# Performance work log

Measured on AMD Instinct MI355X. Metric: run time of the kernel, lower is better.

Reference implementation:

```python
import jax, jax.numpy as jnp
import numpy as np

DT = 0.005
BETA = 0.9
THR = 0.5
TAU_MIN = 0.02
TAU_STEP = 0.03
TAU_R = 0.002
SLOPE = 25.0  # snntorch fast_sigmoid default surrogate slope

@jax.custom_vjp
def spike_fn(x):
    return (x > 0).astype(x.dtype)

def _spike_fwd(x):
    return spike_fn(x), x

def _spike_bwd(x, g):
    return (g / (SLOPE * jnp.abs(x) + 1.0) ** 2,)

spike_fn.defvjp(_spike_fwd, _spike_bwd)

def setup_inputs() -> dict:
    key = jax.random.key(0)
    ks = jax.random.split(key, 8)
    T, NIN, H, NOUT, P = 1000, 4, 4096, 2, 16
    inv_sqrt_h = 1.0 / np.sqrt(H).astype(np.float32)
    return {
        "x": jax.random.normal(ks[0], (T, NIN + 2, 1), jnp.float32),
        "noise": jax.random.normal(ks[1], (T, H, 1), jnp.float32),
        "Win": jax.random.normal(ks[2], (H, NIN + 2), jnp.float32),
        "Wout": jax.random.normal(ks[3], (NOUT, H), jnp.float32) * inv_sqrt_h,
        "pin": jax.random.normal(ks[4], (H, P), jnp.float32) * inv_sqrt_h,
        "pout": jax.random.normal(ks[5], (H, P), jnp.float32) * inv_sqrt_h,
        "l": jax.random.normal(ks[6], (P,), jnp.float32) * inv_sqrt_h,
        "sigmoid_tau_d": jax.random.normal(ks[7], (H, 1), jnp.float32),
    }

def reference(x, noise, Win, Wout, pin, pout, l, sigmoid_tau_d):
    H = Win.shape[0]
    tau_d = jax.nn.sigmoid(sigmoid_tau_d) * TAU_STEP + TAU_MIN   # [H,1]
    Wr = (l * pin) @ pout.T                                      # [H,H] low-rank recurrent matrix
    decay_r = jnp.exp(jnp.asarray(-DT / TAU_R, x.dtype))         # scalar
    decay_d = jnp.exp(-DT / tau_d)                               # [H,1]
    s_gain = DT / (tau_d * TAU_R)                                # [H,1]

    def step(carry, inp):
        mem, r, s = carry
        xi, ni = inp
        I = Win @ xi + Wr @ r + ni / 10.0                        # [H,1]
        # snntorch Leaky, reset_mechanism='subtract': reset from incoming mem (detached)
        reset = jax.lax.stop_gradient(spike_fn(mem - THR))
        mem = BETA * mem + I - reset * THR
        spk = spike_fn(mem - THR)
        s = s * decay_r + s_gain * spk
        r = decay_d * r + DT * s
        return (mem, r, s), r

    z = jnp.zeros((H, 1), x.dtype)
    _, R = jax.lax.scan(step, (z, z, z), (x, noise))             # R: [T,H,1]
    y = jnp.einsum('oh,thj->toj', Wout, R)                       # [T,O,1]
    return y
```

## Files before the change

kernel.cpp:

```cpp
#include <hip/hip_runtime.h>
#include <math.h>

#define KB       4
#define NTHREADS 256
#define NW       4
#define HID      4096
#define HB       (HID / KB)
#define NPT      4
#define TT       1000
#define PP       16
#define SLOTW    32

#define BETA 0.9f
#define THRV 0.5f
#define DTV  0.005f

template<int CTRL>
__device__ __forceinline__ float dppx(float v) {
    return __int_as_float(__builtin_amdgcn_update_dpp(
        0, __float_as_int(v), CTRL, 0xF, 0xF, true));
}

__device__ __forceinline__ unsigned long long AL(const unsigned long long* p) {
    return __hip_atomic_load(p, __ATOMIC_RELAXED, __HIP_MEMORY_SCOPE_AGENT);
}
__device__ __forceinline__ void AS(unsigned long long* p, unsigned long long v) {
    __hip_atomic_store(p, v, __ATOMIC_RELAXED, __HIP_MEMORY_SCOPE_AGENT);
}

__global__ __launch_bounds__(NTHREADS, 1)
void snn_kernel(const float* __restrict__ x,
                const float* __restrict__ noise,
                const float* __restrict__ Win,
                const float* __restrict__ Wout,
                const float* __restrict__ pin,
                const float* __restrict__ pout,
                const float* __restrict__ lvec,
                const float* __restrict__ stdv,
                float* __restrict__ ypart,
                unsigned long long* __restrict__ slots)
{
    const int b    = blockIdx.x;
    const int tid  = threadIdx.x;
    const int wave = tid >> 6;
    const int lane = tid & 63;
    const int h0   = b * HB + tid * NPT;

    const bool lb0 = (lane & 1) != 0;
    const bool lb1 = (lane & 2) != 0;
    const bool lb2 = (lane & 4) != 0;
    const bool lb3 = (lane & 8) != 0;

    const int rbA = (b == 0) ? 1 : 0;
    const int rbB = (b <= 1) ? 2 : 1;
    const int rbC = (b <= 2) ? 3 : 2;

    __shared__ float part[NW][20];
    __shared__ float ubuf[NW][16];

    float lv[PP];
    #pragma unroll
    for (int p = 0; p < PP; p += 4) {
        float4 t4 = *(const float4*)&lvec[p];
        lv[p] = t4.x; lv[p+1] = t4.y; lv[p+2] = t4.z; lv[p+3] = t4.w;
    }
    float pl[NPT][PP], po[NPT][PP];
    #pragma unroll
    for (int j = 0; j < NPT; ++j) {
        #pragma unroll
        for (int p = 0; p < PP; p += 4) {
            float4 a = *(const float4*)&pin[(h0+j)*PP + p];
            pl[j][p]   = a.x*lv[p];   pl[j][p+1] = a.y*lv[p+1];
            pl[j][p+2] = a.z*lv[p+2]; pl[j][p+3] = a.w*lv[p+3];
            float4 e4 = *(const float4*)&pout[(h0+j)*PP + p];
            po[j][p]   = e4.x; po[j][p+1] = e4.y;
            po[j][p+2] = e4.z; po[j][p+3] = e4.w;
        }
    }
    float win[NPT][6];
    #pragma unroll
    for (int j = 0; j < NPT; ++j) {
        const float2* wr = (const float2*)&Win[(h0+j)*6];
        float2 wA = wr[0], wB = wr[1], wC = wr[2];
        win[j][0]=wA.x; win[j][1]=wA.y; win[j][2]=wB.x;
        win[j][3]=wB.y; win[j][4]=wC.x; win[j][5]=wC.y;
    }
    float4 woa = *(const float4*)&Wout[h0];
    float4 wob = *(const float4*)&Wout[HID + h0];

    float4 sd4 = *(const float4*)&stdv[h0];
    float dd[NPT], sg[NPT];
    {
        float sdv[4] = { sd4.x, sd4.y, sd4.z, sd4.w };
        #pragma unroll
        for (int j = 0; j < NPT; ++j) {
            float sig = 1.f / (1.f + expf(-sdv[j]));
            float tau = sig * 0.03f + 0.02f;
            dd[j] = expf(-DTV / tau);
            sg[j] = DTV / (tau * 0.002f);
        }
    }
    const float DECAY_R = expf(-2.5f);
    const float DTE     = DTV * DECAY_R;

    float mem[NPT], rr[NPT], ss[NPT];
    float pre[NPT], rlin[NPT], slin[NPT];
    float palin[PP], yalin = 0.f, yblin = 0.f;
    #pragma unroll
    for (int j = 0; j < NPT; ++j) { mem[j]=0.f; rr[j]=0.f; ss[j]=0.f; }
    #pragma unroll
    for (int p = 0; p < PP; ++p) palin[p] = 0.f;

    const float2* x2 = (const float2*)x;
    float4 nz = *(const float4*)&noise[h0];
    float2 xa = x2[0], xb = x2[1], xc = x2[2];

    float uu[16];
    #pragma unroll
    for (int p = 0; p < 16; ++p) uu[p] = 0.f;

    for (int t = 0; t <= TT; ++t) {
        const int par = t & 1;

        float bs = 0.f;
        if (t > 0) {
            if (lane < 18) {
                bs = (part[0][lane] + part[1][lane])
                   + (part[2][lane] + part[3][lane]);
            }
            if (wave == 0) {
                if (lane < 16) {
                    if (t < TT) {
                        union { float f; unsigned u; } cv; cv.f = bs;
                        unsigned long long pk =
                            ((unsigned long long)(unsigned)t << 32)
                          | (unsigned long long)cv.u;
                        AS(&slots[(size_t)(par*KB + b)*SLOTW + lane], pk);
                    }
                } else if (lane < 18) {
                    ypart[(size_t)b*(2*TT) + (t-1)*2 + (lane-16)] = bs;
                }
            }
        }

        if (t < TT) {
            float nzv[4] = { nz.x, nz.y, nz.z, nz.w };
            #pragma unroll
            for (int j = 0; j < NPT; ++j) {
                float xw = win[j][0]*xa.x + win[j][1]*xa.y
                         + win[j][2]*xb.x + win[j][3]*xb.y
                         + win[j][4]*xc.x + win[j][5]*xc.y;
                float rst = (mem[j] - THRV > 0.f) ? THRV : 0.f;
                pre[j]  = BETA*mem[j] + xw + nzv[j] / 10.0f - rst;
                rlin[j] = dd[j]*rr[j] + DTE*ss[j];
                slin[j] = DECAY_R*ss[j];
            }
            #pragma unroll
            for (int p = 0; p < PP; ++p)
                palin[p] = (po[0][p]*rlin[0] + po[1][p]*rlin[1])
                         + (po[2][p]*rlin[2] + po[3][p]*rlin[3]);
            yalin = (woa.x*rlin[0]+woa.y*rlin[1]) + (woa.z*rlin[2]+woa.w*rlin[3]);
            yblin = (wob.x*rlin[0]+wob.y*rlin[1]) + (wob.z*rlin[2]+wob.w*rlin[3]);
        }

        if (t > 0 && t < TT) {
            const size_t sb = (size_t)par * KB;
            float f0 = 0.f, f1 = 0.f, f2 = 0.f;
            if (lane < 16) {
                const unsigned long long* pa_ = &slots[(sb + rbA)*SLOTW + lane];
                const unsigned long long* pb_ = &slots[(sb + rbB)*SLOTW + lane];
                const unsigned long long* pc_ = &slots[(sb + rbC)*SLOTW + lane];
                unsigned long long va, vb, vc;
                int sp = 0;
                do {
                    va = AL(pa_); vb = AL(pb_); vc = AL(pc_);
                } while ((((unsigned)(va >> 32) != (unsigned)t) |
                          ((unsigned)(vb >> 32) != (unsigned)t) |
                          ((unsigned)(vc >> 32) != (unsigned)t)) &&
                         ++sp < (1 << 20));
                union { unsigned u; float f; } c0, c1, c2;
                c0.u = (unsigned)va; c1.u = (unsigned)vb; c2.u = (unsigned)vc;
                f0 = c0.f; f1 = c1.f; f2 = c2.f;
            }
            float total = (b < 2) ? ((bs + f0) + (f1 + f2))
                                  : ((f0 + f1) + (f2 + bs));
            if (lane < 16) ubuf[wave][lane] = total;
            float4 u0 = *(const float4*)&ubuf[wave][0];
            float4 u1 = *(const float4*)&ubuf[wave][4];
            float4 u2 = *(const float4*)&ubuf[wave][8];
            float4 u3 = *(const float4*)&ubuf[wave][12];
            uu[0]=u0.x; uu[1]=u0.y; uu[2]=u0.z; uu[3]=u0.w;
            uu[4]=u1.x; uu[5]=u1.y; uu[6]=u1.z; uu[7]=u1.w;
            uu[8]=u2.x; uu[9]=u2.y; uu[10]=u2.z; uu[11]=u2.w;
            uu[12]=u3.x; uu[13]=u3.y; uu[14]=u3.z; uu[15]=u3.w;
        }

        if (t < TT) {
            if (t < TT - 1) {
                const int tn = t + 1;
                nz = *(const float4*)&noise[tn * HID + h0];
                xa = x2[tn*3]; xb = x2[tn*3+1]; xc = x2[tn*3+2];
            }

            float rs[NPT];
            #pragma unroll
            for (int j = 0; j < NPT; ++j) {
                float ra  = pl[j][0]*uu[0];
                float rb_ = pl[j][8]*uu[8];
                #pragma unroll
                for (int p = 1; p < 8; ++p) {
                    ra  += pl[j][p]*uu[p];
                    rb_ += pl[j][p+8]*uu[p+8];
                }
                mem[j] = pre[j] + (ra + rb_);
                bool spk = (mem[j] - THRV > 0.f);
                float rspk = spk ? DTV*sg[j] : 0.f;
                ss[j] = slin[j] + (spk ? sg[j] : 0.f);
                rr[j] = rlin[j] + rspk;
                rs[j] = rspk;
            }
            float pa[18];
            #pragma unroll
            for (int p = 0; p < PP; ++p)
                pa[p] = palin[p] + ((po[0][p]*rs[0] + po[1][p]*rs[1])
                                 +  (po[2][p]*rs[2] + po[3][p]*rs[3]));
            pa[16] = yalin + ((woa.x*rs[0]+woa.y*rs[1]) + (woa.z*rs[2]+woa.w*rs[3]));
            pa[17] = yblin + ((wob.x*rs[0]+wob.y*rs[1]) + (wob.z*rs[2]+wob.w*rs[3]));

            float a1[8], yv;
            #pragma unroll
            for (int k = 0; k < 8; ++k) {
                float keep = lb0 ? pa[2*k+1] : pa[2*k];
                float send = lb0 ? pa[2*k]   : pa[2*k+1];
                a1[k] = keep + dppx<0xB1>(send);
            }
            {
                float keep = lb0 ? pa[17] : pa[16];
                float send = lb0 ? pa[16] : pa[17];
                yv = keep + dppx<0xB1>(send);
            }
            float a2[4];
            #pragma unroll
            for (int k = 0; k < 4; ++k) {
                float keep = lb1 ? a1[2*k+1] : a1[2*k];
                float send = lb1 ? a1[2*k]   : a1[2*k+1];
                a2[k] = keep + dppx<0x4E>(send);
            }
            yv += dppx<0x4E>(yv);
            float a3[2];
            #pragma unroll
            for (int k = 0; k < 2; ++k) {
                float keep = lb2 ? a2[2*k+1] : a2[2*k];
                float send = lb2 ? a2[2*k]   : a2[2*k+1];
                a3[k] = keep + __shfl_xor(send, 4, 64);
            }
            yv += __shfl_xor(yv, 4, 64);
            float uv;
            {
                float keep = lb3 ? a3[1] : a3[0];
                float send = lb3 ? a3[0] : a3[1];
                uv = keep + dppx<0x128>(send);
            }
            yv += dppx<0x128>(yv);
            uv += __shfl_xor(uv, 16, 64);
            uv += __shfl_xor(uv, 32, 64);
            yv += __shfl_xor(yv, 16, 64);
            yv += __shfl_xor(yv, 32, 64);

            if (lane < 18) part[wave][lane] = (lane < 16) ? uv : yv;
            __syncthreads();
        }
    }
}

__global__ void ysum_kernel(const float* __restrict__ yp, float* __restrict__ out) {
    int i = blockIdx.x * blockDim.x + threadIdx.x;
    if (i < 2 * TT) {
        float a = yp[i];
        float b = yp[2*TT + i];
        float c = yp[2*2*TT + i];
        float d = yp[3*2*TT + i];
        out[i] = (a + b) + (c + d);
    }
}

extern "C" void kernel_launch(void* const* d_in, const int* in_sizes, int n_in,
                              void* d_out, int out_size, void* d_ws, size_t ws_size,
                              hipStream_t stream)
{
    const float* x     = (const float*)d_in[0];
    const float* noise = (const float*)d_in[1];
    const float* Win   = (const float*)d_in[2];
    const float* Wout  = (const float*)d_in[3];
    const float* pin   = (const float*)d_in[4];
    const float* pout  = (const float*)d_in[5];
    const float* l     = (const float*)d_in[6];
    const float* stdv  = (const float*)d_in[7];
    float* out = (float*)d_out;
    unsigned long long* slots = (unsigned long long*)d_ws;
    float* ypart = (float*)((char*)d_ws + 4096);

    hipLaunchKernelGGL(snn_kernel, dim3(KB), dim3(NTHREADS), 0, stream,
                       x, noise, Win, Wout, pin, pout, l, stdv,
                       ypart, slots);
    hipLaunchKernelGGL(ysum_kernel, dim3((2*TT + 255)/256), dim3(256), 0, stream,
                       ypart, out);
}
```

Measured before the change: 1.611 ms.

## Exchange cross-block partials through L2 with a fallback to device-scope atomics

Launches 32 blocks and keeps only every eighth, so the four working blocks likely land on the same XCD and share an L2. Partial sums are written to two slot arrays: a plain store for L2 and an agent-scope atomic store. Readers poll the L2 copy with a buffer_inv plus plain loads and a bounded spin, and fall back permanently to the atomic copy if that times out. The aim is lower latency per step for the inter-block synchronisation, at the cost of relying on an undocumented block-to-XCD placement and extra stores.

Measured after the change: 1.689 ms. 1.05x slower.

```diff
diff --git a/kernel.cpp b/kernel.cpp
--- a/kernel.cpp
+++ b/kernel.cpp
@@ -2,6 +2,7 @@
 #include <math.h>
 
 #define KB       4
+#define NBOOT    32
 #define NTHREADS 256
 #define NW       4
 #define HID      4096
@@ -26,6 +27,23 @@
 }
 __device__ __forceinline__ void AS(unsigned long long* p, unsigned long long v) {
     __hip_atomic_store(p, v, __ATOMIC_RELAXED, __HIP_MEMORY_SCOPE_AGENT);
+}
+__device__ __forceinline__ void st64_plain(unsigned long long* p, unsigned long long v) {
+    asm volatile("global_store_dwordx2 %0, %1, off" :: "v"(p), "v"(v) : "memory");
+}
+__device__ __forceinline__ void inv_ld3(const unsigned long long* p0,
+                                        const unsigned long long* p1,
+                                        const unsigned long long* p2,
+                                        unsigned long long& v0,
+                                        unsigned long long& v1,
+                                        unsigned long long& v2) {
+    asm volatile("buffer_inv sc0\n\t"
+                 "global_load_dwordx2 %0, %3, off\n\t"
+                 "global_load_dwordx2 %1, %4, off\n\t"
+                 "global_load_dwordx2 %2, %5, off\n\t"
+                 "s_waitcnt vmcnt(0)"
+                 : "=&v"(v0), "=&v"(v1), "=&v"(v2)
+                 : "v"(p0), "v"(p1), "v"(p2) : "memory");
 }
 
 __global__ __launch_bounds__(NTHREADS, 1)
@@ -38,9 +56,12 @@
                 const float* __restrict__ lvec,
                 const float* __restrict__ stdv,
                 float* __restrict__ ypart,
-                unsigned long long* __restrict__ slots)
+                unsigned long long* __restrict__ slotsL2,
+                unsigned long long* __restrict__ slotsAG)
 {
-    const int b    = blockIdx.x;
+    const int bid  = blockIdx.x;
+    if ((bid & 7) != 0) return;
+    const int b    = bid >> 3;
     const int tid  = threadIdx.x;
     const int wave = tid >> 6;
     const int lane = tid & 63;
@@ -119,6 +140,8 @@
     #pragma unroll
     for (int p = 0; p < 16; ++p) uu[p] = 0.f;
 
+    int use_l2 = 1;
+
     for (int t = 0; t <= TT; ++t) {
         const int par = t & 1;
 
@@ -135,7 +158,9 @@
                         unsigned long long pk =
                             ((unsigned long long)(unsigned)t << 32)
                           | (unsigned long long)cv.u;
-                        AS(&slots[(size_t)(par*KB + b)*SLOTW + lane], pk);
+                        const size_t si = (size_t)(par*KB + b)*SLOTW + lane;
+                        st64_plain(&slotsL2[si], pk);
+                        AS(&slotsAG[si], pk);
                     }
                 } else if (lane < 18) {
                     ypart[(size_t)b*(2*TT) + (t-1)*2 + (lane-16)] = bs;
@@ -166,18 +191,40 @@
         if (t > 0 && t < TT) {
             const size_t sb = (size_t)par * KB;
             float f0 = 0.f, f1 = 0.f, f2 = 0.f;
+            unsigned long long va = 0, vb = 0, vc = 0;
+            int got = (lane < 16) ? 0 : 1;
+            if (use_l2) {
+                if (lane < 16) {
+                    const unsigned long long* pa_ = &slotsL2[(sb + rbA)*SLOTW + lane];
+                    const unsigned long long* pb_ = &slotsL2[(sb + rbB)*SLOTW + lane];
+                    const unsigned long long* pc_ = &slotsL2[(sb + rbC)*SLOTW + lane];
+                    const int K = (t == 1) ? 1024 : 64;
+                    int sp = 0, ok;
+                    do {
+                        inv_ld3(pa_, pb_, pc_, va, vb, vc);
+                        ok = ((unsigned)(va >> 32) == (unsigned)t)
+                           & ((unsigned)(vb >> 32) == (unsigned)t)
+                           & ((unsigned)(vc >> 32) == (unsigned)t);
+                    } while (!ok && ++sp < K);
+                    got = ok;
+                }
+                if (!__all(got)) use_l2 = 0;
+            }
+            if (!use_l2) {
+                if (lane < 16 && !got) {
+                    const unsigned long long* pa_ = &slotsAG[(sb + rbA)*SLOTW + lane];
+                    const unsigned long long* pb_ = &slotsAG[(sb + rbB)*SLOTW + lane];
+                    const unsigned long long* pc_ = &slotsAG[(sb + rbC)*SLOTW + lane];
+                    int sp2 = 0;
+                    do {
+                        va = AL(pa_); vb = AL(pb_); vc = AL(pc_);
+                    } while ((((unsigned)(va >> 32) != (unsigned)t) |
+                              ((unsigned)(vb >> 32) != (unsigned)t) |
+                              ((unsigned)(vc >> 32) != (unsigned)t)) &&
+                             ++sp2 < (1 << 20));
+                }
+            }
             if (lane < 16) {
-                const unsigned long long* pa_ = &slots[(sb + rbA)*SLOTW + lane];
-                const unsigned long long* pb_ = &slots[(sb + rbB)*SLOTW + lane];
-                const unsigned long long* pc_ = &slots[(sb + rbC)*SLOTW + lane];
-                unsigned long long va, vb, vc;
-                int sp = 0;
-                do {
-                    va = AL(pa_); vb = AL(pb_); vc = AL(pc_);
-                } while ((((unsigned)(va >> 32) != (unsigned)t) |
-                          ((unsigned)(vb >> 32) != (unsigned)t) |
-                          ((unsigned)(vc >> 32) != (unsigned)t)) &&
-                         ++sp < (1 << 20));
                 union { unsigned u; float f; } c0, c1, c2;
                 c0.u = (unsigned)va; c1.u = (unsigned)vb; c2.u = (unsigned)vc;
                 f0 = c0.f; f1 = c1.f; f2 = c2.f;
@@ -297,12 +344,13 @@
     const float* l     = (const float*)d_in[6];
     const float* stdv  = (const float*)d_in[7];
     float* out = (float*)d_out;
-    unsigned long long* slots = (unsigned long long*)d_ws;
-    float* ypart = (float*)((char*)d_ws + 4096);
-
-    hipLaunchKernelGGL(snn_kernel, dim3(KB), dim3(NTHREADS), 0, stream,
+    unsigned long long* slotsL2 = (unsigned long long*)d_ws;
+    unsigned long long* slotsAG = (unsigned long long*)((char*)d_ws + 4096);
+    float* ypart = (float*)((char*)d_ws + 8192);
+
+    hipLaunchKernelGGL(snn_kernel, dim3(NBOOT), dim3(NTHREADS), 0, stream,
                        x, noise, Win, Wout, pin, pout, l, stdv,
-                       ypart, slots);
+                       ypart, slotsL2, slotsAG);
     hipLaunchKernelGGL(ysum_kernel, dim3((2*TT + 255)/256), dim3(256), 0, stream,
                        ypart, out);
 }
```
